# Optimization experiments

Measured on AMD Instinct MI355X. Metric: run time of the kernel, lower is better.

Reference implementation:

```python
import jax, jax.numpy as jnp
import numpy as np

N = 100_000      # nodes
E = 1_600_000    # edges (before self loops)
IN = 128         # in_dim
HID = 64         # hidden_dim (per head)
HEADS = 2
NEG_SLOPE = 0.2  # PyG GATConv default negative_slope


def setup_inputs() -> dict:
    key = jax.random.key(0)
    k = jax.random.split(key, 6)
    x = jax.random.normal(k[0], (N, IN), jnp.float32)
    edge_index = jax.random.randint(k[1], (2, E), 0, N, dtype=jnp.int64)
    # GATConv linear (no bias in lin, bias added after aggregation in PyG)
    W = jax.random.normal(k[2], (IN, HEADS * HID), jnp.float32) * (1.0 / np.sqrt(IN))
    att_src = jax.random.normal(k[3], (HEADS, HID), jnp.float32) * 0.1
    att_dst = jax.random.normal(k[4], (HEADS, HID), jnp.float32) * 0.1
    bias = jnp.zeros((HEADS * HID,), jnp.float32)
    prelu_w = jnp.full((HEADS * HID,), 0.25, jnp.float32)  # nn.PReLU default init
    return {"x": x, "edge_index": edge_index, "W": W, "att_src": att_src,
            "att_dst": att_dst, "bias": bias, "prelu_w": prelu_w}


def reference(x, edge_index, W, att_src, att_dst, bias, prelu_w):
    n = x.shape[0]
    h = (x @ W).reshape(n, HEADS, HID)                 # [N,H,C]
    a_s = jnp.einsum('nhc,hc->nh', h, att_src)         # [N,H]
    a_d = jnp.einsum('nhc,hc->nh', h, att_dst)         # [N,H]
    # add self loops (PyG default add_self_loops=True)
    loops = jnp.arange(n, dtype=edge_index.dtype)
    src = jnp.concatenate([edge_index[0], loops])      # [Et]
    dst = jnp.concatenate([edge_index[1], loops])      # [Et]
    logits = a_s[src] + a_d[dst]                       # [Et,H]
    logits = jnp.where(logits >= 0, logits, NEG_SLOPE * logits)  # LeakyReLU
    # segment softmax over destination neighborhoods
    m = jax.ops.segment_max(logits, dst, num_segments=n)         # [N,H]
    e = jnp.exp(logits - m[dst])
    s = jax.ops.segment_sum(e, dst, num_segments=n)              # [N,H]
    alpha = e / (s[dst] + 1e-16)                                 # [Et,H]
    # (attention dropout p=0.2 is identity in eval mode)
    msg = h[src] * alpha[..., None]                    # [Et,H,C]
    out = jax.ops.segment_sum(msg, dst, num_segments=n).reshape(n, HEADS * HID)
    out = out + bias
    # PReLU with per-channel weight
    return jnp.where(out >= 0, out, prelu_w * out)
```

## Files before the change

### kernel.cpp

```cpp
#include <hip/hip_runtime.h>
#include <hip/hip_fp16.h>
#include <cstdint>
#include <cstddef>

#define NEG_SLOPE 0.2f
#define BSH 8
#define BNODES 256
#define CAP 5120

typedef __attribute__((ext_vector_type(8))) short short8v;
typedef __attribute__((ext_vector_type(4))) float f32x4;
typedef __attribute__((ext_vector_type(2))) uint32_t u32x2;

__device__ __forceinline__ uint32_t bf16pair(float a, float b) {
    uint32_t ua = __float_as_uint(a), ub = __float_as_uint(b);
    ua = (ua + 0x7fffu + ((ua >> 16) & 1u)) >> 16;
    ub = (ub + 0x7fffu + ((ub >> 16) & 1u)) >> 16;
    return ua | (ub << 16);
}
__device__ __forceinline__ uint16_t rne16(float f) {
    uint32_t u = __float_as_uint(f);
    return (uint16_t)((u + 0x7fffu + ((u >> 16) & 1u)) >> 16);
}
__device__ __forceinline__ float bflo(uint32_t u) { return __uint_as_float(u << 16); }
__device__ __forceinline__ float bfhi(uint32_t u) { return __uint_as_float(u & 0xffff0000u); }
__device__ __forceinline__ uint32_t packf16(float a, float b) {
    __half2 h = __floats2half2_rn(a, b);
    return *reinterpret_cast<uint32_t*>(&h);
}

__global__ __launch_bounds__(256, 3) void gemm_scatter(
    const float* __restrict__ x, const float* __restrict__ W,
    const float* __restrict__ att_src, const float* __restrict__ att_dst,
    uint32_t* __restrict__ hb, float* __restrict__ a_s, float* __restrict__ a_d,
    const int* __restrict__ src, const int* __restrict__ dst,
    int* __restrict__ gcur, uint32_t* __restrict__ pairs,
    int e, int nb, int n, int nbs)
{
    constexpr int PW = 136;
    __shared__ __align__(16) char smem[52224];
    const int tid = threadIdx.x;

    if (blockIdx.x < nbs) {
        int* histL  = (int*)smem;
        int* gbaseL = histL + 512;
        const int t0 = blockIdx.x * 4096;

        for (int i = tid; i < nb; i += 256) histL[i] = 0;
        __syncthreads();

        int      myb[16];
        int      myslot[16];
        uint32_t mypk[16];
#pragma unroll 16
        for (int k = 0; k < 16; ++k) {
            int i = t0 + tid + k * 256;
            if (i < e) {
                int s = __builtin_nontemporal_load(src + i);
                int d = __builtin_nontemporal_load(dst + i);
                int b = d >> BSH;
                myb[k]    = b;
                mypk[k]   = (uint32_t)s | ((uint32_t)(d & (BNODES - 1)) << 17);
                myslot[k] = atomicAdd(&histL[b], 1);
            } else myb[k] = -1;
        }
        __syncthreads();
        for (int i = tid; i < nb; i += 256) {
            int c = histL[i];
            gbaseL[i] = c ? atomicAdd(&gcur[i], c) : 0;
        }
        __syncthreads();
#pragma unroll 16
        for (int k = 0; k < 16; ++k) {
            if (myb[k] >= 0) {
                int p = gbaseL[myb[k]] + myslot[k];
                if (p < CAP) pairs[(size_t)myb[k] * CAP + p] = mypk[k];
            }
        }
        return;
    }

    unsigned short* Wt = (unsigned short*)smem;
    unsigned short* Hs = (unsigned short*)(smem + 34816);
    const int w    = tid >> 6;
    const int lane = tid & 63;
    const int cl   = lane & 15;
    const int gq   = lane >> 4;
    const int base = (blockIdx.x - nbs) * 64;

    const float4* W4 = (const float4*)W;
#pragma unroll
    for (int i = 0; i < 16; ++i) {
        int idx = tid + i * 256;
        int k = idx >> 5, c0 = (idx & 31) * 4;
        float4 v = W4[idx];
        Wt[(c0 + 0) * PW + k] = rne16(v.x);
        Wt[(c0 + 1) * PW + k] = rne16(v.y);
        Wt[(c0 + 2) * PW + k] = rne16(v.z);
        Wt[(c0 + 3) * PW + k] = rne16(v.w);
    }

    float asr[8], adr[8];
#pragma unroll
    for (int t = 0; t < 8; ++t) {
        asr[t] = att_src[t * 16 + cl];
        adr[t] = att_dst[t * 16 + cl];
    }
    __syncthreads();

    const int rowg = base + w * 16 + cl;
    const int rowc = rowg < n ? rowg : (n - 1);
    const f32x4* xp = (const f32x4*)(x + (size_t)rowc * 128);

    f32x4 acc[8];
#pragma unroll
    for (int t = 0; t < 8; ++t) acc[t] = (f32x4){0.f, 0.f, 0.f, 0.f};

#pragma unroll
    for (int s = 0; s < 4; ++s) {
        int kq = s * 8 + gq * 2;
        f32x4 f0 = __builtin_nontemporal_load(xp + kq);
        f32x4 f1 = __builtin_nontemporal_load(xp + kq + 1);
        union { short8v v; uint32_t d[4]; } A;
        A.d[0] = bf16pair(f0.x, f0.y);
        A.d[1] = bf16pair(f0.z, f0.w);
        A.d[2] = bf16pair(f1.x, f1.y);
        A.d[3] = bf16pair(f1.z, f1.w);
#pragma unroll
        for (int t = 0; t < 8; ++t) {
            union { short8v v; uint4 q; } B;
            B.q = *(const uint4*)&Wt[(t * 16 + cl) * PW + s * 32 + gq * 8];
            acc[t] = __builtin_amdgcn_mfma_f32_16x16x32_bf16(A.v, B.v, acc[t], 0, 0, 0);
        }
    }

    float ps0[4], ps1[4], pd0[4], pd1[4];
#pragma unroll
    for (int r = 0; r < 4; ++r) { ps0[r] = ps1[r] = pd0[r] = pd1[r] = 0.f; }
#pragma unroll
    for (int t = 0; t < 8; ++t) {
#pragma unroll
        for (int r = 0; r < 4; ++r) {
            float v = acc[t][r];
            if (t < 4) { ps0[r] = fmaf(v, asr[t], ps0[r]); pd0[r] = fmaf(v, adr[t], pd0[r]); }
            else       { ps1[r] = fmaf(v, asr[t], ps1[r]); pd1[r] = fmaf(v, adr[t], pd1[r]); }
        }
    }
#pragma unroll
    for (int off = 1; off < 16; off <<= 1) {
#pragma unroll
        for (int r = 0; r < 4; ++r) {
            ps0[r] += __shfl_xor(ps0[r], off);
            ps1[r] += __shfl_xor(ps1[r], off);
            pd0[r] += __shfl_xor(pd0[r], off);
            pd1[r] += __shfl_xor(pd1[r], off);
        }
    }
    if (cl == 0) {
#pragma unroll
        for (int r = 0; r < 4; ++r) {
            int rg = base + w * 16 + gq * 4 + r;
            if (rg < n) {
                a_s[rg * 2 + 0] = ps0[r]; a_s[rg * 2 + 1] = ps1[r];
                a_d[rg * 2 + 0] = pd0[r]; a_d[rg * 2 + 1] = pd1[r];
            }
        }
    }

#pragma unroll
    for (int t = 0; t < 8; ++t) {
#pragma unroll
        for (int r = 0; r < 4; ++r) {
            int row = gq * 4 + r;
            Hs[(size_t)w * 16 * PW + row * PW + t * 16 + cl] = rne16(acc[t][r]);
        }
    }
    __syncthreads();
#pragma unroll
    for (int q = 0; q < 4; ++q) {
        int row = q * 4 + gq;
        int cu  = 4 * cl;
        uint4 v = *(const uint4*)&Hs[(size_t)w * 16 * PW + row * PW + cu * 2];
        int rg = base + w * 16 + row;
        if (rg < n) *(uint4*)&hb[(size_t)rg * 64 + cu] = v;
    }
}

__global__ __launch_bounds__(512) void build_csr(
    const uint32_t* __restrict__ pairs, const int* __restrict__ gcur,
    const float* __restrict__ a_s, const float* __restrict__ a_d,
    uint4* __restrict__ meta, uint2* __restrict__ edges, int n, int nb)
{
    __shared__ uint32_t pl[CAP];
    __shared__ int degL[BNODES], curL[BNODES];
    __shared__ float sumL[BNODES * 2];
    __shared__ float adL[BNODES * 2];
    __shared__ int bscan[512];
    __shared__ int wsum8[8];
    const int b = blockIdx.x, tid = threadIdx.x;
    const int lane = tid & 63, wid = tid >> 6;
    const int nbase = b * BNODES;
    const int nodes = min(BNODES, n - nbase);

    int tot = 0;
    if (tid < nb) {
        int nn = min(BNODES, n - tid * BNODES);
        tot = min(gcur[tid], CAP) + nn;
    }
    int sc = tot;
#pragma unroll
    for (int off = 1; off < 64; off <<= 1) {
        int t = __shfl_up(sc, off);
        if (lane >= off) sc += t;
    }
    if (lane == 63) wsum8[wid] = sc;
    __syncthreads();
    {
        int woff = 0;
#pragma unroll
        for (int k = 0; k < 8; ++k) woff += (k < wid) ? wsum8[k] : 0;
        bscan[tid] = sc + woff;
    }
    if (tid < BNODES) degL[tid] = 1;
    float es0 = 0.f, es1 = 0.f;
    if (tid < nodes) {
        int g = nbase + tid;
        float2 ad = ((const float2*)a_d)[g];
        adL[2 * tid]     = ad.x;
        adL[2 * tid + 1] = ad.y;
        float2 as = ((const float2*)a_s)[g];
        float l0 = as.x + ad.x; l0 = l0 >= 0.f ? l0 : NEG_SLOPE * l0;
        float l1 = as.y + ad.y; l1 = l1 >= 0.f ? l1 : NEG_SLOPE * l1;
        es0 = __expf(l0); es1 = __expf(l1);
        sumL[2 * tid] = es0; sumL[2 * tid + 1] = es1;
    }
    __syncthreads();
    const int C    = min(gcur[b], CAP);
    const int base = bscan[b] - (C + nodes);

    for (int i = tid; i < C; i += 512) {
        uint32_t p = __builtin_nontemporal_load(pairs + (size_t)b * CAP + i);
        pl[i] = p;
        atomicAdd(&degL[p >> 17], 1);
    }
    __syncthreads();

    int v = (tid < nodes) ? degL[tid] : 0;
    int sc2 = v;
#pragma unroll
    for (int off = 1; off < 64; off <<= 1) {
        int t = __shfl_up(sc2, off);
        if (lane >= off) sc2 += t;
    }
    if (lane == 63 && tid < BNODES) wsum8[wid] = sc2;
    __syncthreads();
    int woff2 = 0;
#pragma unroll
    for (int k = 0; k < 4; ++k) woff2 += (k < wid) ? wsum8[k] : 0;
    const int exc = sc2 - v + woff2;

    if (tid < nodes) {
        edges[base + exc] = make_uint2((uint32_t)(nbase + tid), packf16(es0, es1));
        curL[tid] = exc + 1;
    }
    __syncthreads();
    for (int i = tid; i < C; i += 512) {
        uint32_t p  = pl[i];
        int dl  = p >> 17;
        int s   = p & 0x1FFFF;
        float2 as = ((const float2*)a_s)[s];
        float l0 = as.x + adL[2 * dl];     l0 = l0 >= 0.f ? l0 : NEG_SLOPE * l0;
        float l1 = as.y + adL[2 * dl + 1]; l1 = l1 >= 0.f ? l1 : NEG_SLOPE * l1;
        float e0 = __expf(l0), e1 = __expf(l1);
        int pos = atomicAdd(&curL[dl], 1);
        edges[base + pos] = make_uint2((uint32_t)s, packf16(e0, e1));
        atomicAdd(&sumL[2 * dl],     e0);
        atomicAdd(&sumL[2 * dl + 1], e1);
    }
    __syncthreads();
    if (tid < nodes) {
        uint4 m;
        m.x = (uint32_t)(base + exc);
        m.y = (uint32_t)v;
        m.z = __float_as_uint(1.f / (sumL[2 * tid]     + 1e-16f));
        m.w = __float_as_uint(1.f / (sumL[2 * tid + 1] + 1e-16f));
        meta[nbase + tid] = m;
    }
}

__global__ __launch_bounds__(256) void attn_agg(
    const uint32_t* __restrict__ hb, const uint2* __restrict__ edges,
    const uint4* __restrict__ meta,
    const float* __restrict__ bias, const float* __restrict__ prelu_w,
    float* __restrict__ out, int n)
{
    const int gw   = (blockIdx.x * blockDim.x + threadIdx.x) >> 6;
    const int lane = threadIdx.x & 63;
    if (gw >= n) return;
    const uint4 mt  = meta[gw];
    const int start = (int)mt.x;
    const int deg   = (int)mt.y;
    const float inv0 = __uint_as_float(mt.z);
    const float inv1 = __uint_as_float(mt.w);

    if (deg <= 64) {
        int sv = 0; float al0 = 0.f, al1 = 0.f;
        if (lane < deg) {
            u32x2 ed = __builtin_nontemporal_load((const u32x2*)(edges + start + lane));
            sv = (int)ed.x;
            uint32_t ey = ed.y;
            __half2 h2 = *reinterpret_cast<__half2*>(&ey);
            al0 = __half2float(__low2half(h2))  * inv0;
            al1 = __half2float(__high2half(h2)) * inv1;
        }
        const int g = lane >> 4, r = lane & 15;
        float acc[8];
#pragma unroll
        for (int q = 0; q < 8; ++q) acc[q] = 0.f;
        const uint4* hb4 = (const uint4*)hb;

        if (deg <= 16) {
            float Aj[4]; uint4 q[4];
#pragma unroll
            for (int k = 0; k < 4; ++k) {
                int j = g + 4 * k;
                int s = __shfl(sv, j);
                float A0 = __shfl(al0, j), A1 = __shfl(al1, j);
                Aj[k] = (r < 8) ? A0 : A1;
                q[k] = hb4[(size_t)s * 16 + r];
            }
#pragma unroll
            for (int k = 0; k < 4; ++k) {
                acc[0] = fmaf(Aj[k], bflo(q[k].x), acc[0]);
                acc[1] = fmaf(Aj[k], bfhi(q[k].x), acc[1]);
                acc[2] = fmaf(Aj[k], bflo(q[k].y), acc[2]);
                acc[3] = fmaf(Aj[k], bfhi(q[k].y), acc[3]);
                acc[4] = fmaf(Aj[k], bflo(q[k].z), acc[4]);
                acc[5] = fmaf(Aj[k], bfhi(q[k].z), acc[5]);
                acc[6] = fmaf(Aj[k], bflo(q[k].w), acc[6]);
                acc[7] = fmaf(Aj[k], bfhi(q[k].w), acc[7]);
            }
        } else if (deg <= 32) {
            float Aj[8]; uint4 q[8];
#pragma unroll
            for (int k = 0; k < 8; ++k) {
                int j = g + 4 * k;
                int s = __shfl(sv, j);
                float A0 = __shfl(al0, j), A1 = __shfl(al1, j);
                Aj[k] = (r < 8) ? A0 : A1;
                q[k] = hb4[(size_t)s * 16 + r];
            }
#pragma unroll
            for (int k = 0; k < 8; ++k) {
                acc[0] = fmaf(Aj[k], bflo(q[k].x), acc[0]);
                acc[1] = fmaf(Aj[k], bfhi(q[k].x), acc[1]);
                acc[2] = fmaf(Aj[k], bflo(q[k].y), acc[2]);
                acc[3] = fmaf(Aj[k], bfhi(q[k].y), acc[3]);
                acc[4] = fmaf(Aj[k], bflo(q[k].z), acc[4]);
                acc[5] = fmaf(Aj[k], bfhi(q[k].z), acc[5]);
                acc[6] = fmaf(Aj[k], bflo(q[k].w), acc[6]);
                acc[7] = fmaf(Aj[k], bfhi(q[k].w), acc[7]);
            }
        } else {
            const int iters = (deg + 15) >> 4;
            for (int jj = 0; jj < iters; ++jj) {
                float Aj[4]; uint4 q[4];
#pragma unroll
                for (int k = 0; k < 4; ++k) {
                    int j = jj * 16 + g + 4 * k;
                    int s = __shfl(sv, j);
                    float A0 = __shfl(al0, j), A1 = __shfl(al1, j);
                    Aj[k] = (r < 8) ? A0 : A1;
                    q[k] = hb4[(size_t)s * 16 + r];
                }
#pragma unroll
                for (int k = 0; k < 4; ++k) {
                    acc[0] = fmaf(Aj[k], bflo(q[k].x), acc[0]);
                    acc[1] = fmaf(Aj[k], bfhi(q[k].x), acc[1]);
                    acc[2] = fmaf(Aj[k], bflo(q[k].y), acc[2]);
                    acc[3] = fmaf(Aj[k], bfhi(q[k].y), acc[3]);
                    acc[4] = fmaf(Aj[k], bflo(q[k].z), acc[4]);
                    acc[5] = fmaf(Aj[k], bfhi(q[k].z), acc[5]);
                    acc[6] = fmaf(Aj[k], bflo(q[k].w), acc[6]);
                    acc[7] = fmaf(Aj[k], bfhi(q[k].w), acc[7]);
                }
            }
        }
#pragma unroll
        for (int q = 0; q < 8; ++q) {
            acc[q] += __shfl_xor(acc[q], 16);
            acc[q] += __shfl_xor(acc[q], 32);
        }
        if (lane < 16) {
            float4 b0 = ((const float4*)bias)[lane * 2];
            float4 b1 = ((const float4*)bias)[lane * 2 + 1];
            float4 p0 = ((const float4*)prelu_w)[lane * 2];
            float4 p1 = ((const float4*)prelu_w)[lane * 2 + 1];
            f32x4 w0, w1;
            w0.x = acc[0] + b0.x; w0.x = w0.x >= 0.f ? w0.x : p0.x * w0.x;
            w0.y = acc[1] + b0.y; w0.y = w0.y >= 0.f ? w0.y : p0.y * w0.y;
            w0.z = acc[2] + b0.z; w0.z = w0.z >= 0.f ? w0.z : p0.z * w0.z;
            w0.w = acc[3] + b0.w; w0.w = w0.w >= 0.f ? w0.w : p0.w * w0.w;
            w1.x = acc[4] + b1.x; w1.x = w1.x >= 0.f ? w1.x : p1.x * w1.x;
            w1.y = acc[5] + b1.y; w1.y = w1.y >= 0.f ? w1.y : p1.y * w1.y;
            w1.z = acc[6] + b1.z; w1.z = w1.z >= 0.f ? w1.z : p1.z * w1.z;
            w1.w = acc[7] + b1.w; w1.w = w1.w >= 0.f ? w1.w : p1.w * w1.w;
            float* op = out + (size_t)gw * 128 + lane * 8;
            __builtin_nontemporal_store(w0, (f32x4*)op);
            __builtin_nontemporal_store(w1, (f32x4*)(op + 4));
        }
    } else {
        float accL = 0.f, accH = 0.f;
        for (int t0 = 0; t0 < deg; t0 += 64) {
            int tt = t0 + lane;
            int sv = 0; float al0 = 0.f, al1 = 0.f;
            if (tt < deg) {
                uint2 ed = edges[start + tt];
                sv = (int)ed.x;
                __half2 h2 = *reinterpret_cast<__half2*>(&ed.y);
                al0 = __half2float(__low2half(h2))  * inv0;
                al1 = __half2float(__high2half(h2)) * inv1;
            }
            int kmax = min(64, deg - t0);
            for (int j = 0; j < kmax; ++j) {
                int   s  = __shfl(sv, j);
                float A0 = __shfl(al0, j);
                float A1 = __shfl(al1, j);
                float A  = (lane < 32) ? A0 : A1;
                uint32_t u = hb[(size_t)s * 64 + lane];
                accL = fmaf(A, bflo(u), accL);
                accH = fmaf(A, bfhi(u), accH);
            }
        }
        float2 bz = ((const float2*)bias)[lane];
        float2 pw = ((const float2*)prelu_w)[lane];
        float o0 = accL + bz.x, o1 = accH + bz.y;
        o0 = o0 >= 0.f ? o0 : pw.x * o0;
        o1 = o1 >= 0.f ? o1 : pw.y * o1;
        float2 rr; rr.x = o0; rr.y = o1;
        ((float2*)out)[(size_t)gw * 64 + lane] = rr;
    }
}

extern "C" void kernel_launch(void* const* d_in, const int* in_sizes, int n_in,
                              void* d_out, int out_size, void* d_ws, size_t ws_size,
                              hipStream_t stream)
{
    const float* x        = (const float*)d_in[0];
    const int*   ei       = (const int*)d_in[1];
    const float* W        = (const float*)d_in[2];
    const float* att_src  = (const float*)d_in[3];
    const float* att_dst  = (const float*)d_in[4];
    const float* bias     = (const float*)d_in[5];
    const float* prelu_w  = (const float*)d_in[6];
    float* out = (float*)d_out;

    const int n = in_sizes[0] / 128;
    const int e = in_sizes[1] / 2;
    const int* srcp = ei;
    const int* dstp = ei + e;
    const int nb  = (n + BNODES - 1) / BNODES;
    const int nbs = (e + 4095) / 4096;
    const int nbg = (n + 63) / 64;

    uint32_t* hb    = (uint32_t*)d_ws;
    uint4*    meta  = (uint4*)(hb + (size_t)n * 64);
    float*    a_s   = (float*)(meta + n);
    float*    a_d   = a_s + (size_t)n * 2;
    int*      gcur  = (int*)(a_d + (size_t)n * 2);
    uint32_t* pairs = (uint32_t*)(gcur + 512);
    uint2*    edges = (uint2*)(pairs + (size_t)nb * CAP);

    hipMemsetAsync(gcur, 0, 512 * sizeof(int), stream);
    gemm_scatter<<<nbs + nbg, 256, 0, stream>>>(x, W, att_src, att_dst,
                                                hb, a_s, a_d, srcp, dstp,
                                                gcur, pairs, e, nb, n, nbs);
    build_csr<<<nb, 512, 0, stream>>>(pairs, gcur, a_s, a_d, meta, edges, n, nb);
    attn_agg<<<(n + 3) / 4, 256, 0, stream>>>(hb, edges, meta, bias, prelu_w, out, n);
}
```

Before: 159.3 us.

## Fuse CSR build and attention aggregation into one kernel using LDS

Merges build_csr and attn_agg into a single kernel. Each 1024-thread block builds its 256-node CSR slice (columns and exp weights) in shared memory and then aggregates those nodes directly, 16 nodes per wave. This removes the global edges/meta round trip, the cross-block prefix scan and one launch. In exchange each block now holds large LDS buffers, which limits occupancy, and only about 391 blocks are launched. The specialized low-degree paths (<=16, <=32) are also dropped in favour of the generic 16-per-iteration loop.

```diff
diff --git a/kernel.cpp b/kernel.cpp
--- a/kernel.cpp
+++ b/kernel.cpp
@@ -10,7 +10,6 @@
 
 typedef __attribute__((ext_vector_type(8))) short short8v;
 typedef __attribute__((ext_vector_type(4))) float f32x4;
-typedef __attribute__((ext_vector_type(2))) uint32_t u32x2;
 
 __device__ __forceinline__ uint32_t bf16pair(float a, float b) {
     uint32_t ua = __float_as_uint(a), ub = __float_as_uint(b);
@@ -186,43 +185,27 @@
     }
 }
 
-__global__ __launch_bounds__(512) void build_csr(
+__global__ __launch_bounds__(1024, 2) void build_agg(
     const uint32_t* __restrict__ pairs, const int* __restrict__ gcur,
     const float* __restrict__ a_s, const float* __restrict__ a_d,
-    uint4* __restrict__ meta, uint2* __restrict__ edges, int n, int nb)
+    const uint32_t* __restrict__ hb,
+    const float* __restrict__ bias, const float* __restrict__ prelu_w,
+    float* __restrict__ out, int n)
 {
-    __shared__ uint32_t pl[CAP];
-    __shared__ int degL[BNODES], curL[BNODES];
+    __shared__ uint32_t colL[CAP + BNODES];
+    __shared__ uint32_t eL[CAP + BNODES];
+    __shared__ int degL[BNODES], curL[BNODES], rpL[BNODES];
     __shared__ float sumL[BNODES * 2];
     __shared__ float adL[BNODES * 2];
-    __shared__ int bscan[512];
-    __shared__ int wsum8[8];
+    __shared__ int wsum[16];
     const int b = blockIdx.x, tid = threadIdx.x;
     const int lane = tid & 63, wid = tid >> 6;
     const int nbase = b * BNODES;
     const int nodes = min(BNODES, n - nbase);
-
-    int tot = 0;
-    if (tid < nb) {
-        int nn = min(BNODES, n - tid * BNODES);
-        tot = min(gcur[tid], CAP) + nn;
-    }
-    int sc = tot;
-#pragma unroll
-    for (int off = 1; off < 64; off <<= 1) {
-        int t = __shfl_up(sc, off);
-        if (lane >= off) sc += t;
-    }
-    if (lane == 63) wsum8[wid] = sc;
-    __syncthreads();
-    {
-        int woff = 0;
-#pragma unroll
-        for (int k = 0; k < 8; ++k) woff += (k < wid) ? wsum8[k] : 0;
-        bscan[tid] = sc + woff;
-    }
+    const int C     = min(gcur[b], CAP);
+
+    float es0 = 0.f, es1 = 0.f;
     if (tid < BNODES) degL[tid] = 1;
-    float es0 = 0.f, es1 = 0.f;
     if (tid < nodes) {
         int g = nbase + tid;
         float2 ad = ((const float2*)a_d)[g];
@@ -235,133 +218,88 @@
         sumL[2 * tid] = es0; sumL[2 * tid + 1] = es1;
     }
     __syncthreads();
-    const int C    = min(gcur[b], CAP);
-    const int base = bscan[b] - (C + nodes);
-
-    for (int i = tid; i < C; i += 512) {
-        uint32_t p = __builtin_nontemporal_load(pairs + (size_t)b * CAP + i);
-        pl[i] = p;
-        atomicAdd(&degL[p >> 17], 1);
-    }
-    __syncthreads();
-
-    int v = (tid < nodes) ? degL[tid] : 0;
-    int sc2 = v;
-#pragma unroll
-    for (int off = 1; off < 64; off <<= 1) {
-        int t = __shfl_up(sc2, off);
-        if (lane >= off) sc2 += t;
-    }
-    if (lane == 63 && tid < BNODES) wsum8[wid] = sc2;
-    __syncthreads();
-    int woff2 = 0;
-#pragma unroll
-    for (int k = 0; k < 4; ++k) woff2 += (k < wid) ? wsum8[k] : 0;
-    const int exc = sc2 - v + woff2;
-
+
+    for (int i = tid; i < C; i += 1024)
+        atomicAdd(&degL[pairs[(size_t)b * CAP + i] >> 17], 1);
+    __syncthreads();
+
+    int v = 0, exc = 0;
+    if (tid < BNODES) {
+        v = (tid < nodes) ? degL[tid] : 0;
+        int sc = v;
+#pragma unroll
+        for (int off = 1; off < 64; off <<= 1) {
+            int t = __shfl_up(sc, off);
+            if (lane >= off) sc += t;
+        }
+        if (lane == 63) wsum[wid] = sc;
+        exc = sc - v;
+    }
+    __syncthreads();
     if (tid < nodes) {
-        edges[base + exc] = make_uint2((uint32_t)(nbase + tid), packf16(es0, es1));
+        int woff = 0;
+#pragma unroll
+        for (int k = 0; k < 4; ++k) woff += (k < wid) ? wsum[k] : 0;
+        exc += woff;
+        rpL[tid]  = exc;
         curL[tid] = exc + 1;
-    }
-    __syncthreads();
-    for (int i = tid; i < C; i += 512) {
-        uint32_t p  = pl[i];
-        int dl  = p >> 17;
-        int s   = p & 0x1FFFF;
+        colL[exc] = (uint32_t)(nbase + tid);
+        eL[exc]   = packf16(es0, es1);
+    }
+    __syncthreads();
+
+    for (int i = tid; i < C; i += 1024) {
+        uint32_t p = pairs[(size_t)b * CAP + i];
+        int dl = p >> 17;
+        int s  = p & 0x1FFFF;
         float2 as = ((const float2*)a_s)[s];
         float l0 = as.x + adL[2 * dl];     l0 = l0 >= 0.f ? l0 : NEG_SLOPE * l0;
         float l1 = as.y + adL[2 * dl + 1]; l1 = l1 >= 0.f ? l1 : NEG_SLOPE * l1;
         float e0 = __expf(l0), e1 = __expf(l1);
         int pos = atomicAdd(&curL[dl], 1);
-        edges[base + pos] = make_uint2((uint32_t)s, packf16(e0, e1));
+        colL[pos] = (uint32_t)s;
+        eL[pos]   = packf16(e0, e1);
         atomicAdd(&sumL[2 * dl],     e0);
         atomicAdd(&sumL[2 * dl + 1], e1);
     }
     __syncthreads();
     if (tid < nodes) {
-        uint4 m;
-        m.x = (uint32_t)(base + exc);
-        m.y = (uint32_t)v;
-        m.z = __float_as_uint(1.f / (sumL[2 * tid]     + 1e-16f));
-        m.w = __float_as_uint(1.f / (sumL[2 * tid + 1] + 1e-16f));
-        meta[nbase + tid] = m;
-    }
-}
-
-__global__ __launch_bounds__(256) void attn_agg(
-    const uint32_t* __restrict__ hb, const uint2* __restrict__ edges,
-    const uint4* __restrict__ meta,
-    const float* __restrict__ bias, const float* __restrict__ prelu_w,
-    float* __restrict__ out, int n)
-{
-    const int gw   = (blockIdx.x * blockDim.x + threadIdx.x) >> 6;
-    const int lane = threadIdx.x & 63;
-    if (gw >= n) return;
-    const uint4 mt  = meta[gw];
-    const int start = (int)mt.x;
-    const int deg   = (int)mt.y;
-    const float inv0 = __uint_as_float(mt.z);
-    const float inv1 = __uint_as_float(mt.w);
-
-    if (deg <= 64) {
-        int sv = 0; float al0 = 0.f, al1 = 0.f;
-        if (lane < deg) {
-            u32x2 ed = __builtin_nontemporal_load((const u32x2*)(edges + start + lane));
-            sv = (int)ed.x;
-            uint32_t ey = ed.y;
-            __half2 h2 = *reinterpret_cast<__half2*>(&ey);
-            al0 = __half2float(__low2half(h2))  * inv0;
-            al1 = __half2float(__high2half(h2)) * inv1;
-        }
-        const int g = lane >> 4, r = lane & 15;
-        float acc[8];
-#pragma unroll
-        for (int q = 0; q < 8; ++q) acc[q] = 0.f;
-        const uint4* hb4 = (const uint4*)hb;
-
-        if (deg <= 16) {
-            float Aj[4]; uint4 q[4];
-#pragma unroll
-            for (int k = 0; k < 4; ++k) {
-                int j = g + 4 * k;
-                int s = __shfl(sv, j);
-                float A0 = __shfl(al0, j), A1 = __shfl(al1, j);
-                Aj[k] = (r < 8) ? A0 : A1;
-                q[k] = hb4[(size_t)s * 16 + r];
-            }
-#pragma unroll
-            for (int k = 0; k < 4; ++k) {
-                acc[0] = fmaf(Aj[k], bflo(q[k].x), acc[0]);
-                acc[1] = fmaf(Aj[k], bfhi(q[k].x), acc[1]);
-                acc[2] = fmaf(Aj[k], bflo(q[k].y), acc[2]);
-                acc[3] = fmaf(Aj[k], bfhi(q[k].y), acc[3]);
-                acc[4] = fmaf(Aj[k], bflo(q[k].z), acc[4]);
-                acc[5] = fmaf(Aj[k], bfhi(q[k].z), acc[5]);
-                acc[6] = fmaf(Aj[k], bflo(q[k].w), acc[6]);
-                acc[7] = fmaf(Aj[k], bfhi(q[k].w), acc[7]);
-            }
-        } else if (deg <= 32) {
-            float Aj[8]; uint4 q[8];
-#pragma unroll
-            for (int k = 0; k < 8; ++k) {
-                int j = g + 4 * k;
-                int s = __shfl(sv, j);
-                float A0 = __shfl(al0, j), A1 = __shfl(al1, j);
-                Aj[k] = (r < 8) ? A0 : A1;
-                q[k] = hb4[(size_t)s * 16 + r];
-            }
-#pragma unroll
-            for (int k = 0; k < 8; ++k) {
-                acc[0] = fmaf(Aj[k], bflo(q[k].x), acc[0]);
-                acc[1] = fmaf(Aj[k], bfhi(q[k].x), acc[1]);
-                acc[2] = fmaf(Aj[k], bflo(q[k].y), acc[2]);
-                acc[3] = fmaf(Aj[k], bfhi(q[k].y), acc[3]);
-                acc[4] = fmaf(Aj[k], bflo(q[k].z), acc[4]);
-                acc[5] = fmaf(Aj[k], bfhi(q[k].z), acc[5]);
-                acc[6] = fmaf(Aj[k], bflo(q[k].w), acc[6]);
-                acc[7] = fmaf(Aj[k], bfhi(q[k].w), acc[7]);
-            }
-        } else {
+        sumL[2 * tid]     = 1.f / (sumL[2 * tid]     + 1e-16f);
+        sumL[2 * tid + 1] = 1.f / (sumL[2 * tid + 1] + 1e-16f);
+    }
+    __syncthreads();
+
+    const int g = lane >> 4, r = lane & 15;
+    const uint4* hb4 = (const uint4*)hb;
+    float4 b0, b1, p0, p1;
+    if (lane < 16) {
+        b0 = ((const float4*)bias)[lane * 2];
+        b1 = ((const float4*)bias)[lane * 2 + 1];
+        p0 = ((const float4*)prelu_w)[lane * 2];
+        p1 = ((const float4*)prelu_w)[lane * 2 + 1];
+    }
+
+    for (int k2 = 0; k2 < 16; ++k2) {
+        const int ln = wid * 16 + k2;
+        if (ln >= nodes) break;
+        const int startL = rpL[ln];
+        const int deg    = degL[ln];
+        const float inv0 = sumL[2 * ln];
+        const float inv1 = sumL[2 * ln + 1];
+        const int gid    = nbase + ln;
+
+        if (deg <= 64) {
+            int sv = 0; float al0 = 0.f, al1 = 0.f;
+            if (lane < deg) {
+                sv = (int)colL[startL + lane];
+                uint32_t ey = eL[startL + lane];
+                __half2 h2 = *reinterpret_cast<__half2*>(&ey);
+                al0 = __half2float(__low2half(h2))  * inv0;
+                al1 = __half2float(__high2half(h2)) * inv1;
+            }
+            float acc[8];
+#pragma unroll
+            for (int q = 0; q < 8; ++q) acc[q] = 0.f;
             const int iters = (deg + 15) >> 4;
             for (int jj = 0; jj < iters; ++jj) {
                 float Aj[4]; uint4 q[4];
@@ -385,60 +323,56 @@
                     acc[7] = fmaf(Aj[k], bfhi(q[k].w), acc[7]);
                 }
             }
-        }
-#pragma unroll
-        for (int q = 0; q < 8; ++q) {
-            acc[q] += __shfl_xor(acc[q], 16);
-            acc[q] += __shfl_xor(acc[q], 32);
-        }
-        if (lane < 16) {
-            float4 b0 = ((const float4*)bias)[lane * 2];
-            float4 b1 = ((const float4*)bias)[lane * 2 + 1];
-            float4 p0 = ((const float4*)prelu_w)[lane * 2];
-            float4 p1 = ((const float4*)prelu_w)[lane * 2 + 1];
-            f32x4 w0, w1;
-            w0.x = acc[0] + b0.x; w0.x = w0.x >= 0.f ? w0.x : p0.x * w0.x;
-            w0.y = acc[1] + b0.y; w0.y = w0.y >= 0.f ? w0.y : p0.y * w0.y;
-            w0.z = acc[2] + b0.z; w0.z = w0.z >= 0.f ? w0.z : p0.z * w0.z;
-            w0.w = acc[3] + b0.w; w0.w = w0.w >= 0.f ? w0.w : p0.w * w0.w;
-            w1.x = acc[4] + b1.x; w1.x = w1.x >= 0.f ? w1.x : p1.x * w1.x;
-            w1.y = acc[5] + b1.y; w1.y = w1.y >= 0.f ? w1.y : p1.y * w1.y;
-            w1.z = acc[6] + b1.z; w1.z = w1.z >= 0.f ? w1.z : p1.z * w1.z;
-            w1.w = acc[7] + b1.w; w1.w = w1.w >= 0.f ? w1.w : p1.w * w1.w;
-            float* op = out + (size_t)gw * 128 + lane * 8;
-            __builtin_nontemporal_store(w0, (f32x4*)op);
-            __builtin_nontemporal_store(w1, (f32x4*)(op + 4));
-        }
-    } else {
-        float accL = 0.f, accH = 0.f;
-        for (int t0 = 0; t0 < deg; t0 += 64) {
-            int tt = t0 + lane;
-            int sv = 0; float al0 = 0.f, al1 = 0.f;
-            if (tt < deg) {
-                uint2 ed = edges[start + tt];
-                sv = (int)ed.x;
-                __half2 h2 = *reinterpret_cast<__half2*>(&ed.y);
-                al0 = __half2float(__low2half(h2))  * inv0;
-                al1 = __half2float(__high2half(h2)) * inv1;
-            }
-            int kmax = min(64, deg - t0);
-            for (int j = 0; j < kmax; ++j) {
-                int   s  = __shfl(sv, j);
-                float A0 = __shfl(al0, j);
-                float A1 = __shfl(al1, j);
-                float A  = (lane < 32) ? A0 : A1;
-                uint32_t u = hb[(size_t)s * 64 + lane];
-                accL = fmaf(A, bflo(u), accL);
-                accH = fmaf(A, bfhi(u), accH);
-            }
-        }
-        float2 bz = ((const float2*)bias)[lane];
-        float2 pw = ((const float2*)prelu_w)[lane];
-        float o0 = accL + bz.x, o1 = accH + bz.y;
-        o0 = o0 >= 0.f ? o0 : pw.x * o0;
-        o1 = o1 >= 0.f ? o1 : pw.y * o1;
-        float2 rr; rr.x = o0; rr.y = o1;
-        ((float2*)out)[(size_t)gw * 64 + lane] = rr;
+#pragma unroll
+            for (int q = 0; q < 8; ++q) {
+                acc[q] += __shfl_xor(acc[q], 16);
+                acc[q] += __shfl_xor(acc[q], 32);
+            }
+            if (lane < 16) {
+                f32x4 w0, w1;
+                w0.x = acc[0] + b0.x; w0.x = w0.x >= 0.f ? w0.x : p0.x * w0.x;
+                w0.y = acc[1] + b0.y; w0.y = w0.y >= 0.f ? w0.y : p0.y * w0.y;
+                w0.z = acc[2] + b0.z; w0.z = w0.z >= 0.f ? w0.z : p0.z * w0.z;
+                w0.w = acc[3] + b0.w; w0.w = w0.w >= 0.f ? w0.w : p0.w * w0.w;
+                w1.x = acc[4] + b1.x; w1.x = w1.x >= 0.f ? w1.x : p1.x * w1.x;
+                w1.y = acc[5] + b1.y; w1.y = w1.y >= 0.f ? w1.y : p1.y * w1.y;
+                w1.z = acc[6] + b1.z; w1.z = w1.z >= 0.f ? w1.z : p1.z * w1.z;
+                w1.w = acc[7] + b1.w; w1.w = w1.w >= 0.f ? w1.w : p1.w * w1.w;
+                float* op = out + (size_t)gid * 128 + lane * 8;
+                __builtin_nontemporal_store(w0, (f32x4*)op);
+                __builtin_nontemporal_store(w1, (f32x4*)(op + 4));
+            }
+        } else {
+            float accL = 0.f, accH = 0.f;
+            for (int t0 = 0; t0 < deg; t0 += 64) {
+                int tt = t0 + lane;
+                int sv = 0; float al0 = 0.f, al1 = 0.f;
+                if (tt < deg) {
+                    sv = (int)colL[startL + tt];
+                    uint32_t ey = eL[startL + tt];
+                    __half2 h2 = *reinterpret_cast<__half2*>(&ey);
+                    al0 = __half2float(__low2half(h2))  * inv0;
+                    al1 = __half2float(__high2half(h2)) * inv1;
+                }
+                int kmax = min(64, deg - t0);
+                for (int j = 0; j < kmax; ++j) {
+                    int   s  = __shfl(sv, j);
+                    float A0 = __shfl(al0, j);
+                    float A1 = __shfl(al1, j);
+                    float A  = (lane < 32) ? A0 : A1;
+                    uint32_t u = hb[(size_t)s * 64 + lane];
+                    accL = fmaf(A, bflo(u), accL);
+                    accH = fmaf(A, bfhi(u), accH);
+                }
+            }
+            float2 bz = ((const float2*)bias)[lane];
+            float2 pw = ((const float2*)prelu_w)[lane];
+            float o0 = accL + bz.x, o1 = accH + bz.y;
+            o0 = o0 >= 0.f ? o0 : pw.x * o0;
+            o1 = o1 >= 0.f ? o1 : pw.y * o1;
+            float2 rr; rr.x = o0; rr.y = o1;
+            ((float2*)out)[(size_t)gid * 64 + lane] = rr;
+        }
     }
 }
 
@@ -464,17 +398,15 @@
     const int nbg = (n + 63) / 64;
 
     uint32_t* hb    = (uint32_t*)d_ws;
-    uint4*    meta  = (uint4*)(hb + (size_t)n * 64);
-    float*    a_s   = (float*)(meta + n);
+    float*    a_s   = (float*)(hb + (size_t)n * 64);
     float*    a_d   = a_s + (size_t)n * 2;
     int*      gcur  = (int*)(a_d + (size_t)n * 2);
     uint32_t* pairs = (uint32_t*)(gcur + 512);
-    uint2*    edges = (uint2*)(pairs + (size_t)nb * CAP);
 
     hipMemsetAsync(gcur, 0, 512 * sizeof(int), stream);
     gemm_scatter<<<nbs + nbg, 256, 0, stream>>>(x, W, att_src, att_dst,
                                                 hb, a_s, a_d, srcp, dstp,
                                                 gcur, pairs, e, nb, n, nbs);
-    build_csr<<<nb, 512, 0, stream>>>(pairs, gcur, a_s, a_d, meta, edges, n, nb);
-    attn_agg<<<(n + 3) / 4, 256, 0, stream>>>(hb, edges, meta, bias, prelu_w, out, n);
-}
+    build_agg<<<nb, 1024, 0, stream>>>(pairs, gcur, a_s, a_d, hb,
+                                       bias, prelu_w, out, n);
+}
```

Result: slower. 162.6 us (+2.0%).
